# Kernel optimization log

Hardware: AMD Instinct MI355X
Metric: run time of the kernel (lower is better)

The kernel has to match this reference:

```python
import jax, jax.numpy as jnp
import numpy as np

EPS = 1e-7  # K.epsilon()


def setup_inputs() -> dict:
    key = jax.random.key(0)
    k1, k2, k3 = jax.random.split(key, 3)
    B, T, D = 32, 2048, 1024
    one = jax.random.normal(k1, (B, D), dtype=jnp.float32)
    many = jax.random.normal(k2, (B, T, D), dtype=jnp.float32)
    W = jax.random.normal(k3, (D, D), dtype=jnp.float32) * (1.0 / np.sqrt(D))
    return {"one": one, "many": many, "W": W}


def reference(one, many, W):
    # logits = batch_dot(tanh(many @ W), one, axes=[2,1]) -> [B, T]
    proj = jnp.tanh(jnp.einsum('btd,de->bte', many, W))       # [B,T,D]
    logits = jnp.einsum('btd,bd->bt', proj, one)               # [B,T]
    # stable softmax with Keras epsilon in denominator
    ai = jnp.exp(logits - jnp.max(logits, axis=-1, keepdims=True))
    att_weights = ai / (jnp.sum(ai, axis=-1, keepdims=True) + EPS)  # [B,T]
    result = jnp.einsum('btd,bt->bd', many, att_weights)       # [B,D]
    return result, att_weights
```

## Files before the change

kernel.cpp:

```cpp
#include <hip/hip_runtime.h>
#include <hip/hip_bf16.h>

typedef _Float16 half8v __attribute__((ext_vector_type(8)));
typedef __fp16  fp16x2 __attribute__((ext_vector_type(2)));
typedef float floatx4 __attribute__((ext_vector_type(4)));

#define NB 32
#define NT 2048
#define ND 1024
#define NM (NB * NT)

#define GL16(g, l)                                                             \
    __builtin_amdgcn_global_load_lds(                                          \
        (const __attribute__((address_space(1))) void*)(g),                    \
        (__attribute__((address_space(3))) void*)(l), 16, 0, 0)

__device__ __forceinline__ float fast_tanh(float x) {
    x = fminf(9.0f, fmaxf(-9.0f, x));
    float e = __builtin_amdgcn_exp2f(x * 2.8853900817779268f);
    return (e - 1.0f) * __builtin_amdgcn_rcpf(e + 1.0f);
}

__global__ __launch_bounds__(256)
void wt_kernel(const float* __restrict__ W, _Float16* __restrict__ Wt) {
    __shared__ float tile[32][33];
    int tx = threadIdx.x, ty = threadIdx.y;
    int bx = blockIdx.x, by = blockIdx.y;
    #pragma unroll
    for (int i = 0; i < 4; ++i) {
        int y = by * 32 + ty + i * 8;
        tile[ty + i * 8][tx] = W[y * ND + bx * 32 + tx];
    }
    __syncthreads();
    #pragma unroll
    for (int i = 0; i < 4; ++i) {
        int e = bx * 32 + ty + i * 8;
        Wt[e * ND + by * 32 + tx] = (_Float16)tile[tx][ty + i * 8];
    }
}

__global__ __launch_bounds__(256)
void conv_kernel(const float* __restrict__ many, _Float16* __restrict__ manyh) {
    size_t idx = ((size_t)blockIdx.x * 256 + threadIdx.x) * 8;
    size_t stride = (size_t)gridDim.x * 256 * 8;
    for (size_t i = idx; i < (size_t)NM * ND; i += stride) {
        float4 a = *reinterpret_cast<const float4*>(many + i);
        float4 b = *reinterpret_cast<const float4*>(many + i + 4);
        union { _Float16 h[8]; uint4 u; } o;
        o.h[0] = (_Float16)a.x; o.h[1] = (_Float16)a.y;
        o.h[2] = (_Float16)a.z; o.h[3] = (_Float16)a.w;
        o.h[4] = (_Float16)b.x; o.h[5] = (_Float16)b.y;
        o.h[6] = (_Float16)b.z; o.h[7] = (_Float16)b.w;
        *reinterpret_cast<uint4*>(manyh + i) = o.u;
    }
}

__global__ __launch_bounds__(256, 4)
void gemm_logits_s(const _Float16* __restrict__ manyh, const _Float16* __restrict__ Wt,
                   const float* __restrict__ one, float* __restrict__ logits) {
    __shared__ uint4 LDSQ[2048];
    char* Ld = (char*)LDSQ;

    int bid = blockIdx.x;
    int j = (bid & 7) * 512 + (bid >> 3);
    int mb = j >> 3, nb = j & 7;
    int m0 = mb * 128, n0 = nb * 128;

    int tid = threadIdx.x;
    int lane = tid & 63, w = tid >> 6;
    int wr = w >> 1, wc = w & 1;
    int l15 = lane & 15, l4 = lane >> 4;

    const char* aS = (const char*)manyh + ((size_t)(m0 + (tid >> 3)) << 11)
                   + (size_t)(((tid & 7) ^ ((tid >> 3) & 7)) << 4);
    const char* bS = (const char*)Wt + ((size_t)(n0 + (tid >> 3)) << 11)
                   + (size_t)(((tid & 7) ^ ((tid >> 3) & 7)) << 4);

    floatx4 acc[4][4] = {};

    #pragma unroll 1
    for (int kb = 0; kb < 1024; kb += 64) {
        #pragma unroll
        for (int i = 0; i < 4; ++i)
            GL16(aS + kb * 2 + i * 65536, Ld + i * 4096 + tid * 16);
        #pragma unroll
        for (int i = 0; i < 4; ++i)
            GL16(bS + kb * 2 + i * 65536, Ld + 16384 + i * 4096 + tid * 16);
        __syncthreads();

        #pragma unroll
        for (int ks = 0; ks < 64; ks += 32) {
            half8v af[4], bf[4];
            #pragma unroll
            for (int mi = 0; mi < 4; ++mi) {
                int r = wr * 64 + mi * 16 + l15;
                int c = (ks >> 3) + l4;
                af[mi] = *(const half8v*)(Ld + r * 128 + ((c ^ (r & 7)) << 4));
            }
            #pragma unroll
            for (int ni = 0; ni < 4; ++ni) {
                int r = wc * 64 + ni * 16 + l15;
                int c = (ks >> 3) + l4;
                bf[ni] = *(const half8v*)(Ld + 16384 + r * 128 + ((c ^ (r & 7)) << 4));
            }
            #pragma unroll
            for (int mi = 0; mi < 4; ++mi)
                #pragma unroll
                for (int ni = 0; ni < 4; ++ni)
                    acc[mi][ni] = __builtin_amdgcn_mfma_f32_16x16x32_f16(
                        af[mi], bf[ni], acc[mi][ni], 0, 0, 0);
        }
        __syncthreads();
    }

    int bidx = m0 >> 11;
    float onev[4];
    #pragma unroll
    for (int ni = 0; ni < 4; ++ni)
        onev[ni] = one[(bidx << 10) + n0 + wc * 64 + ni * 16 + l15];

    #pragma unroll
    for (int mi = 0; mi < 4; ++mi) {
        float part[4] = {0.f, 0.f, 0.f, 0.f};
        #pragma unroll
        for (int ni = 0; ni < 4; ++ni)
            #pragma unroll
            for (int b = 0; b < 4; ++b)
                part[b] += fast_tanh(acc[mi][ni][b]) * onev[ni];
        #pragma unroll
        for (int off = 1; off < 16; off <<= 1)
            #pragma unroll
            for (int b = 0; b < 4; ++b)
                part[b] += __shfl_xor(part[b], off, 64);
        #pragma unroll
        for (int b = 0; b < 4; ++b)
            if (l15 == mi * 4 + b)
                atomicAdd(&logits[m0 + wr * 64 + mi * 16 + l4 * 4 + b], part[b]);
    }
}

__global__ __launch_bounds__(256, 2)
void gemm_logits(const float* __restrict__ many, const _Float16* __restrict__ Wt,
                 const float* __restrict__ one, float* __restrict__ logits) {
    __shared__ uint4 AsQ[2048];
    __shared__ uint4 BsQ[1024];
    char* AsB = (char*)AsQ;
    char* BsB = (char*)BsQ;

    int bid = blockIdx.x;
    int j = (bid & 7) * 512 + (bid >> 3);
    int mb = j >> 3, nb = j & 7;
    int m0 = mb * 128, n0 = nb * 128;

    int tid = threadIdx.x;
    int lane = tid & 63, w = tid >> 6;
    int wr = w >> 1, wc = w & 1;
    int l15 = lane & 15, l4 = lane >> 4;

    const char* aS = (const char*)many + ((size_t)(m0 + (tid >> 4)) << 12)
        + (size_t)(((tid & 15) ^ ((tid >> 4) & 7)) << 4);
    const char* bS = (const char*)Wt + ((size_t)(n0 + (tid >> 3)) << 11)
        + (size_t)(((tid & 7) ^ ((tid >> 3) & 7)) << 4);
    char* aD = AsB + tid * 16;
    char* bD = BsB + tid * 16;

    floatx4 acc[4][4] = {};

    for (int kb = 0; kb < 1024; kb += 64) {
        #pragma unroll
        for (int i = 0; i < 8; ++i)
            GL16(aS + kb * 4 + i * 65536, aD + i * 4096);
        #pragma unroll
        for (int i = 0; i < 4; ++i)
            GL16(bS + kb * 2 + i * 65536, bD + i * 4096);
        __syncthreads();

        #pragma unroll
        for (int ks = 0; ks < 64; ks += 32) {
            half8v af[4], bf[4];
            #pragma unroll
            for (int mi = 0; mi < 4; ++mi) {
                int r = wr * 64 + mi * 16 + l15;
                int s = l15 & 7;
                const char* base = AsB + r * 256;
                int c0 = (ks >> 2) + l4 * 2;
                float4 x = *(const float4*)(base + (size_t)((c0 ^ s) << 4));
                float4 y = *(const float4*)(base + (size_t)(((c0 + 1) ^ s) << 4));
                union { fp16x2 p[4]; half8v h; } u;
                u.p[0] = __builtin_amdgcn_cvt_pkrtz(x.x, x.y);
                u.p[1] = __builtin_amdgcn_cvt_pkrtz(x.z, x.w);
                u.p[2] = __builtin_amdgcn_cvt_pkrtz(y.x, y.y);
                u.p[3] = __builtin_amdgcn_cvt_pkrtz(y.z, y.w);
                af[mi] = u.h;
            }
            #pragma unroll
            for (int ni = 0; ni < 4; ++ni) {
                int r = wc * 64 + ni * 16 + l15;
                int s = l15 & 7;
                int c = (ks >> 3) + l4;
                bf[ni] = *(const half8v*)(BsB + r * 128 + (size_t)((c ^ s) << 4));
            }
            #pragma unroll
            for (int mi = 0; mi < 4; ++mi)
                #pragma unroll
                for (int ni = 0; ni < 4; ++ni)
                    acc[mi][ni] = __builtin_amdgcn_mfma_f32_16x16x32_f16(
                        af[mi], bf[ni], acc[mi][ni], 0, 0, 0);
        }
        __syncthreads();
    }

    int bidx = m0 >> 11;
    float onev[4];
    #pragma unroll
    for (int ni = 0; ni < 4; ++ni)
        onev[ni] = one[(bidx << 10) + n0 + wc * 64 + ni * 16 + l15];

    #pragma unroll
    for (int mi = 0; mi < 4; ++mi) {
        float part[4] = {0.f, 0.f, 0.f, 0.f};
        #pragma unroll
        for (int ni = 0; ni < 4; ++ni)
            #pragma unroll
            for (int b = 0; b < 4; ++b)
                part[b] += fast_tanh(acc[mi][ni][b]) * onev[ni];
        #pragma unroll
        for (int off = 1; off < 16; off <<= 1)
            #pragma unroll
            for (int b = 0; b < 4; ++b)
                part[b] += __shfl_xor(part[b], off, 64);
        #pragma unroll
        for (int b = 0; b < 4; ++b)
            if (l15 == mi * 4 + b)
                atomicAdd(&logits[m0 + wr * 64 + mi * 16 + l4 * 4 + b], part[b]);
    }
}

__global__ __launch_bounds__(256)
void softmax_kernel(const float* __restrict__ logits, float* __restrict__ att) {
    int b = blockIdx.x, tid = threadIdx.x;
    const float* lr = logits + (b << 11);
    float lv[8];
    float mx = -1e30f;
    #pragma unroll
    for (int i = 0; i < 8; ++i) { lv[i] = lr[tid + (i << 8)]; mx = fmaxf(mx, lv[i]); }
    #pragma unroll
    for (int off = 1; off < 64; off <<= 1) mx = fmaxf(mx, __shfl_xor(mx, off, 64));
    __shared__ float redm[4];
    __shared__ float reds[4];
    int wv = tid >> 6;
    if ((tid & 63) == 0) redm[wv] = mx;
    __syncthreads();
    mx = fmaxf(fmaxf(redm[0], redm[1]), fmaxf(redm[2], redm[3]));
    float s = 0.f;
    #pragma unroll
    for (int i = 0; i < 8; ++i) { lv[i] = expf(lv[i] - mx); s += lv[i]; }
    #pragma unroll
    for (int off = 1; off < 64; off <<= 1) s += __shfl_xor(s, off, 64);
    if ((tid & 63) == 0) reds[wv] = s;
    __syncthreads();
    s = reds[0] + reds[1] + reds[2] + reds[3];
    float inv = 1.0f / (s + 1e-7f);
    #pragma unroll
    for (int i = 0; i < 8; ++i) att[(b << 11) + tid + (i << 8)] = lv[i] * inv;
}

__global__ __launch_bounds__(256)
void out_kernel_h(const _Float16* __restrict__ manyh, const float* __restrict__ att,
                  float* __restrict__ out) {
    int b = blockIdx.x >> 4, tch = blockIdx.x & 15;
    int tid = threadIdx.x;
    __shared__ float aw[128];
    if (tid < 128) aw[tid] = att[(b << 11) + tch * 128 + tid];
    __syncthreads();
    const _Float16* mp = manyh + (((size_t)b * NT + tch * 128) << 10) + tid * 4;
    float a0 = 0.f, a1 = 0.f, a2 = 0.f, a3 = 0.f;
    for (int t = 0; t < 128; ++t) {
        float wgt = aw[t];
        union { _Float16 h[4]; uint2 u; } v;
        v.u = *reinterpret_cast<const uint2*>(mp + ((size_t)t << 10));
        a0 = fmaf((float)v.h[0], wgt, a0); a1 = fmaf((float)v.h[1], wgt, a1);
        a2 = fmaf((float)v.h[2], wgt, a2); a3 = fmaf((float)v.h[3], wgt, a3);
    }
    float* op = out + (b << 10) + tid * 4;
    atomicAdd(op + 0, a0); atomicAdd(op + 1, a1);
    atomicAdd(op + 2, a2); atomicAdd(op + 3, a3);
}

__global__ __launch_bounds__(256)
void out_kernel(const float* __restrict__ many, const float* __restrict__ att,
                float* __restrict__ out) {
    int b = blockIdx.x >> 4, tch = blockIdx.x & 15;
    int tid = threadIdx.x;
    __shared__ float aw[128];
    if (tid < 128) aw[tid] = att[(b << 11) + tch * 128 + tid];
    __syncthreads();
    const float* mp = many + (((size_t)b * NT + tch * 128) << 10) + tid * 4;
    float ax = 0.f, ay = 0.f, az = 0.f, aww = 0.f;
    for (int t = 0; t < 128; ++t) {
        float wgt = aw[t];
        float4 v = *reinterpret_cast<const float4*>(mp + ((size_t)t << 10));
        ax = fmaf(v.x, wgt, ax); ay = fmaf(v.y, wgt, ay);
        az = fmaf(v.z, wgt, az); aww = fmaf(v.w, wgt, aww);
    }
    float* op = out + (b << 10) + tid * 4;
    atomicAdd(op + 0, ax); atomicAdd(op + 1, ay);
    atomicAdd(op + 2, az); atomicAdd(op + 3, aww);
}

extern "C" void kernel_launch(void* const* d_in, const int* in_sizes, int n_in,
                              void* d_out, int out_size, void* d_ws, size_t ws_size,
                              hipStream_t stream) {
    const float* one  = (const float*)d_in[0];
    const float* many = (const float*)d_in[1];
    const float* W    = (const float*)d_in[2];
    float* out = (float*)d_out;

    size_t wtB = (size_t)ND * ND * 2;
    size_t lgB = (size_t)NM * 4;
    size_t mhB = (size_t)NM * ND * 2;
    _Float16* Wt    = (_Float16*)d_ws;
    float*    logits = (float*)((char*)d_ws + wtB);
    _Float16* manyh = (_Float16*)((char*)d_ws + wtB + lgB);
    float*    att   = out + NB * ND;
    bool big = ws_size >= wtB + lgB + mhB;

    (void)hipMemsetAsync(out, 0, (size_t)NB * ND * sizeof(float), stream);
    (void)hipMemsetAsync(logits, 0, (size_t)NM * sizeof(float), stream);

    wt_kernel<<<dim3(32, 32), dim3(32, 8), 0, stream>>>(W, Wt);
    if (big) {
        conv_kernel<<<2048, 256, 0, stream>>>(many, manyh);
        gemm_logits_s<<<4096, 256, 0, stream>>>(manyh, Wt, one, logits);
    } else {
        gemm_logits<<<4096, 256, 0, stream>>>(many, Wt, one, logits);
    }
    softmax_kernel<<<NB, 256, 0, stream>>>(logits, att);
    if (big) out_kernel_h<<<NB * 16, 256, 0, stream>>>(manyh, att, out);
    else     out_kernel<<<NB * 16, 256, 0, stream>>>(many, att, out);
}
```

Before: 250.3 us.

## Fuse fp32-to-fp16 conversion of many into the logits GEMM A-tile load

Removes the separate conversion pass over many. The GEMM now reads fp32 rows directly, converts them to fp16 in registers and stores them to LDS, and blocks with nb==0 also write the fp16 copy for the later weighted-sum kernel. This avoids a full extra read and write of the large tensor, but the A-tile now goes through synchronous register loads instead of async global-to-LDS copies, and 8x more fp32 traffic is re-read across the column blocks. The two memsets are also replaced by a single zeroing kernel, and the fallback kernel's occupancy hint is raised.

```diff
diff --git a/kernel.cpp b/kernel.cpp
--- a/kernel.cpp
+++ b/kernel.cpp
@@ -22,6 +22,13 @@
 }
 
 __global__ __launch_bounds__(256)
+void zero_kernel(float* __restrict__ out, float* __restrict__ logits) {
+    int i = blockIdx.x * 256 + threadIdx.x;
+    logits[i] = 0.f;
+    if (i < NB * ND) out[i] = 0.f;
+}
+
+__global__ __launch_bounds__(256)
 void wt_kernel(const float* __restrict__ W, _Float16* __restrict__ Wt) {
     __shared__ float tile[32][33];
     int tx = threadIdx.x, ty = threadIdx.y;
@@ -39,25 +46,10 @@
     }
 }
 
-__global__ __launch_bounds__(256)
-void conv_kernel(const float* __restrict__ many, _Float16* __restrict__ manyh) {
-    size_t idx = ((size_t)blockIdx.x * 256 + threadIdx.x) * 8;
-    size_t stride = (size_t)gridDim.x * 256 * 8;
-    for (size_t i = idx; i < (size_t)NM * ND; i += stride) {
-        float4 a = *reinterpret_cast<const float4*>(many + i);
-        float4 b = *reinterpret_cast<const float4*>(many + i + 4);
-        union { _Float16 h[8]; uint4 u; } o;
-        o.h[0] = (_Float16)a.x; o.h[1] = (_Float16)a.y;
-        o.h[2] = (_Float16)a.z; o.h[3] = (_Float16)a.w;
-        o.h[4] = (_Float16)b.x; o.h[5] = (_Float16)b.y;
-        o.h[6] = (_Float16)b.z; o.h[7] = (_Float16)b.w;
-        *reinterpret_cast<uint4*>(manyh + i) = o.u;
-    }
-}
-
 __global__ __launch_bounds__(256, 4)
-void gemm_logits_s(const _Float16* __restrict__ manyh, const _Float16* __restrict__ Wt,
-                   const float* __restrict__ one, float* __restrict__ logits) {
+void gemm_logits_f(const float* __restrict__ many, const _Float16* __restrict__ Wt,
+                   const float* __restrict__ one, float* __restrict__ logits,
+                   _Float16* __restrict__ manyh) {
     __shared__ uint4 LDSQ[2048];
     char* Ld = (char*)LDSQ;
 
@@ -71,8 +63,13 @@
     int wr = w >> 1, wc = w & 1;
     int l15 = lane & 15, l4 = lane >> 4;
 
-    const char* aS = (const char*)manyh + ((size_t)(m0 + (tid >> 3)) << 11)
-                   + (size_t)(((tid & 7) ^ ((tid >> 3) & 7)) << 4);
+    int arow = tid >> 3, cc = tid & 7;
+    int akey = arow & 7;
+    const char* aSrc = (const char*)many + ((size_t)(m0 + arow) << 12) + cc * 32;
+    char*       mhD  = (char*)manyh + ((size_t)(m0 + arow) << 11) + cc * 16;
+    char*       aD   = Ld + arow * 128 + ((cc ^ akey) << 4);
+    bool wrH = (nb == 0);
+
     const char* bS = (const char*)Wt + ((size_t)(n0 + (tid >> 3)) << 11)
                    + (size_t)(((tid & 7) ^ ((tid >> 3) & 7)) << 4);
 
@@ -82,10 +79,19 @@
     for (int kb = 0; kb < 1024; kb += 64) {
         #pragma unroll
         for (int i = 0; i < 4; ++i)
-            GL16(aS + kb * 2 + i * 65536, Ld + i * 4096 + tid * 16);
-        #pragma unroll
-        for (int i = 0; i < 4; ++i)
             GL16(bS + kb * 2 + i * 65536, Ld + 16384 + i * 4096 + tid * 16);
+        #pragma unroll
+        for (int i = 0; i < 4; ++i) {
+            float4 x = *(const float4*)(aSrc + (size_t)i * 131072 + kb * 4);
+            float4 y = *(const float4*)(aSrc + (size_t)i * 131072 + kb * 4 + 16);
+            union { fp16x2 p[4]; uint4 u; } o;
+            o.p[0] = __builtin_amdgcn_cvt_pkrtz(x.x, x.y);
+            o.p[1] = __builtin_amdgcn_cvt_pkrtz(x.z, x.w);
+            o.p[2] = __builtin_amdgcn_cvt_pkrtz(y.x, y.y);
+            o.p[3] = __builtin_amdgcn_cvt_pkrtz(y.z, y.w);
+            *(uint4*)(aD + i * 4096) = o.u;
+            if (wrH) *(uint4*)(mhD + (size_t)i * 65536 + kb * 2) = o.u;
+        }
         __syncthreads();
 
         #pragma unroll
@@ -139,7 +145,7 @@
     }
 }
 
-__global__ __launch_bounds__(256, 2)
+__global__ __launch_bounds__(256, 3)
 void gemm_logits(const float* __restrict__ many, const _Float16* __restrict__ Wt,
                  const float* __restrict__ one, float* __restrict__ logits) {
     __shared__ uint4 AsQ[2048];
@@ -319,23 +325,21 @@
     size_t wtB = (size_t)ND * ND * 2;
     size_t lgB = (size_t)NM * 4;
     size_t mhB = (size_t)NM * ND * 2;
-    _Float16* Wt    = (_Float16*)d_ws;
+    _Float16* Wt     = (_Float16*)d_ws;
     float*    logits = (float*)((char*)d_ws + wtB);
-    _Float16* manyh = (_Float16*)((char*)d_ws + wtB + lgB);
-    float*    att   = out + NB * ND;
+    _Float16* manyh  = (_Float16*)((char*)d_ws + wtB + lgB);
+    float*    att    = out + NB * ND;
     bool big = ws_size >= wtB + lgB + mhB;
 
-    (void)hipMemsetAsync(out, 0, (size_t)NB * ND * sizeof(float), stream);
-    (void)hipMemsetAsync(logits, 0, (size_t)NM * sizeof(float), stream);
-
+    zero_kernel<<<256, 256, 0, stream>>>(out, logits);
     wt_kernel<<<dim3(32, 32), dim3(32, 8), 0, stream>>>(W, Wt);
     if (big) {
-        conv_kernel<<<2048, 256, 0, stream>>>(many, manyh);
-        gemm_logits_s<<<4096, 256, 0, stream>>>(manyh, Wt, one, logits);
+        gemm_logits_f<<<4096, 256, 0, stream>>>(many, Wt, one, logits, manyh);
+        softmax_kernel<<<NB, 256, 0, stream>>>(logits, att);
+        out_kernel_h<<<NB * 16, 256, 0, stream>>>(manyh, att, out);
     } else {
         gemm_logits<<<4096, 256, 0, stream>>>(many, Wt, one, logits);
-    }
-    softmax_kernel<<<NB, 256, 0, stream>>>(logits, att);
-    if (big) out_kernel_h<<<NB * 16, 256, 0, stream>>>(manyh, att, out);
-    else     out_kernel<<<NB * 16, 256, 0, stream>>>(many, att, out);
-}
+        softmax_kernel<<<NB, 256, 0, stream>>>(logits, att);
+        out_kernel<<<NB * 16, 256, 0, stream>>>(many, att, out);
+    }
+}
```

New measurement: 295.4 us. 18.0% more time.
